# Optimization experiments

Measured on AMD Instinct MI355X. Metric: run time of the kernel, lower is better.

Reference implementation:

```python
import jax, jax.numpy as jnp
import numpy as np

B, T, H, P, ND = 32768, 128, 32, 7, 8
TEMPERATURE = 1.0
EPS = 1e-20


def setup_inputs() -> dict:
    key = jax.random.key(0)
    ks = jax.random.split(key, 12)
    sc = 0.1
    return {
        "h_n": jax.random.normal(ks[0], (1, B, H), dtype=jnp.float32),
        "c_n": jax.random.normal(ks[1], (1, B, H), dtype=jnp.float32),
        "noise": jax.random.normal(ks[2], (B, ND), dtype=jnp.float32),
        "gumbel_u": jax.random.uniform(ks[3], (T, B, P), dtype=jnp.float32),
        "W_init": jax.random.normal(ks[4], (H, H + ND), dtype=jnp.float32) * sc,
        "b_init": jnp.zeros((H,), dtype=jnp.float32),
        "W_ih": jax.random.normal(ks[5], (4 * H, P), dtype=jnp.float32) * sc,
        "W_hh": jax.random.normal(ks[6], (4 * H, H), dtype=jnp.float32) * sc,
        "b_ih": jnp.zeros((4 * H,), dtype=jnp.float32),
        "b_hh": jnp.zeros((4 * H,), dtype=jnp.float32),
        "W_head": jax.random.normal(ks[7], (P, H), dtype=jnp.float32) * sc,
        "b_head": jnp.zeros((P,), dtype=jnp.float32),
        "future_length": T,
    }


def reference(h_n, c_n, noise, gumbel_u, W_init, b_init, W_ih, W_hh, b_ih, b_hh, W_head, b_head, future_length):
    # fc_init on [h_n ; noise]
    h0 = jnp.concatenate([h_n[0], noise], axis=1) @ W_init.T + b_init  # (B, H)
    c0 = c_n[0]  # (B, H)
    nP = W_head.shape[0]
    y0 = jnp.zeros((h0.shape[0], nP), dtype=h0.dtype)

    def step(carry, u):
        h, c, y = carry
        # torch LSTM gate order: i, f, g, o
        gates = y @ W_ih.T + b_ih + h @ W_hh.T + b_hh  # (B, 4H)
        i, f, g, o = jnp.split(gates, 4, axis=-1)
        c = jax.nn.sigmoid(f) * c + jax.nn.sigmoid(i) * jnp.tanh(g)
        h = jax.nn.sigmoid(o) * jnp.tanh(c)
        logits = h @ W_head.T + b_head  # (B, P)
        # Gumbel-softmax (training, hard=True, straight-through)
        gnoise = -jnp.log(-jnp.log(u + EPS) + EPS)
        y_soft = jax.nn.softmax((logits + gnoise) / TEMPERATURE, axis=-1)
        y_hard = jax.nn.one_hot(jnp.argmax(y_soft, axis=-1), nP, dtype=y_soft.dtype)
        y = jax.lax.stop_gradient(y_hard - y_soft) + y_soft
        return (h, c, y), (logits, y)

    _, (logits_t, samples_t) = jax.lax.scan(step, (h0, c0, y0), gumbel_u)
    # (T, B, P) -> (B, T, P)
    return jnp.swapaxes(logits_t, 0, 1), jnp.swapaxes(samples_t, 0, 1)
```

## Files before the change

### kernel.cpp

```cpp
#include <hip/hip_runtime.h>


#define Hh 32
#define Pp 7
#define NDd 8

typedef float f32x2 __attribute__((ext_vector_type(2)));

static __device__ __forceinline__ f32x2 fma2(f32x2 w, float h, f32x2 a) {
  return __builtin_elementwise_fma(w, (f32x2){h, h}, a);
}

__global__ void gumbel_noise_kernel(const float4* __restrict__ u,
                                    float4* __restrict__ o, int n4) {
  int i = blockIdx.x * blockDim.x + threadIdx.x;
  int stride = gridDim.x * blockDim.x;
  for (; i < n4; i += stride) {
    float4 v = u[i];
    float4 r;
    r.x = -logf(-logf(v.x + 1e-20f) + 1e-20f);
    r.y = -logf(-logf(v.y + 1e-20f) + 1e-20f);
    r.z = -logf(-logf(v.z + 1e-20f) + 1e-20f);
    r.w = -logf(-logf(v.w + 1e-20f) + 1e-20f);
    o[i] = r;
  }
}

template <int PRE>
__global__ __launch_bounds__(64, 4) void gen_decoder_kernel(
    const float* __restrict__ h_n, const float* __restrict__ c_n,
    const float* __restrict__ noise, const float* __restrict__ gsrc,
    const float* __restrict__ W_init, const float* __restrict__ b_init,
    const float* __restrict__ W_ih, const float* __restrict__ W_hh,
    const float* __restrict__ b_ih, const float* __restrict__ b_hh,
    const float* __restrict__ W_head, const float* __restrict__ b_head,
    float* __restrict__ out, int B, int T)
{
  __shared__ f32x2 sTIG[8 * 32];
  __shared__ f32x2 sTFO[8 * 32];
  __shared__ __align__(16) float sm_h[2 * 36];
  __shared__ __align__(16) float smL[2][56];
  __shared__ __align__(16) float smS[2][56];

  const int l    = threadIdx.x;
  const int half = l >> 5;
  const int j    = l & 31;
  const int b    = blockIdx.x * 2 + half;

  for (int i = l; i < 8 * 32; i += 64) {
    int k = i >> 5, jj = i & 31;
    float vi = b_ih[jj]      + b_hh[jj]      + ((k < 7) ? W_ih[jj * 7 + k]        : 0.f);
    float vf = b_ih[32 + jj] + b_hh[32 + jj] + ((k < 7) ? W_ih[(32 + jj) * 7 + k] : 0.f);
    float vg = b_ih[64 + jj] + b_hh[64 + jj] + ((k < 7) ? W_ih[(64 + jj) * 7 + k] : 0.f);
    float vo = b_ih[96 + jj] + b_hh[96 + jj] + ((k < 7) ? W_ih[(96 + jj) * 7 + k] : 0.f);
    sTIG[i] = (f32x2){vi, vg};
    sTFO[i] = (f32x2){vf, vo};
  }

  {
    float x[Hh + NDd];
#pragma unroll
    for (int i = 0; i < 8; i++)
      ((float4*)x)[i] = *(const float4*)&h_n[(size_t)b * Hh + 4 * i];
    ((float4*)x)[8] = *(const float4*)&noise[(size_t)b * NDd];
    ((float4*)x)[9] = *(const float4*)&noise[(size_t)b * NDd + 4];
    float a = b_init[j];
    const float* wr = &W_init[j * (Hh + NDd)];
#pragma unroll
    for (int k = 0; k < Hh + NDd; k++) a = fmaf(wr[k], x[k], a);
    sm_h[half * 36 + j] = a;
  }
  float c = c_n[(size_t)b * Hh + j];

  f32x2 wPK[32];
  {
    const float* WA = W_hh + (size_t)l * Hh;
    const float* WB = W_hh + (size_t)(l + 64) * Hh;
#pragma unroll
    for (int kc = 0; kc < 8; kc++) {
      float4 wa = *(const float4*)&WA[4 * kc];
      float4 wb = *(const float4*)&WB[4 * kc];
      wPK[4 * kc + 0] = (f32x2){wa.x, wb.x};
      wPK[4 * kc + 1] = (f32x2){wa.y, wb.y};
      wPK[4 * kc + 2] = (f32x2){wa.z, wb.z};
      wPK[4 * kc + 3] = (f32x2){wa.w, wb.w};
    }
  }
  const f32x2* tbl = half ? sTFO : sTIG;

  const int hp = (l & 31) >> 2;
  const int hq = l & 3;
  float whead[8];
  float bh = 0.f;
  if (hp < 7) {
#pragma unroll
    for (int m = 0; m < 8; m++) whead[m] = W_head[hp * Hh + hq + 4 * m];
    bh = b_head[hp];
  } else {
#pragma unroll
    for (int m = 0; m < 8; m++) whead[m] = 0.f;
  }

  const int r7 = l & 7;
  const int cpc = (r7 < 7) ? r7 : 6;
  const float* gL = gsrc + (size_t)b * Pp + cpc;
  const size_t strideT = (size_t)B * Pp;
  const size_t SOFF = (size_t)B * T * Pp;

  int kA = 7, kB = 7;
  float* outL = out + (size_t)b * T * Pp;

  for (int t = 0; t < T; ++t) {
    float nv;
    if constexpr (PRE) {
      nv = gL[(size_t)t * strideT];
    } else {
      float uv = gL[(size_t)t * strideT];
      nv = -logf(-logf(uv + 1e-20f) + 1e-20f);
    }

    f32x2 accA = tbl[(kA << 5) + j];
    f32x2 accB = tbl[(kB << 5) + j];
#pragma unroll
    for (int kc = 0; kc < 8; kc++) {
      float4 hvA = *(const float4*)&sm_h[4 * kc];
      float4 hvB = *(const float4*)&sm_h[36 + 4 * kc];
      accA = fma2(wPK[4 * kc + 0], hvA.x, accA);
      accB = fma2(wPK[4 * kc + 0], hvB.x, accB);
      accA = fma2(wPK[4 * kc + 1], hvA.y, accA);
      accB = fma2(wPK[4 * kc + 1], hvB.y, accB);
      accA = fma2(wPK[4 * kc + 2], hvA.z, accA);
      accB = fma2(wPK[4 * kc + 2], hvB.z, accB);
      accA = fma2(wPK[4 * kc + 3], hvA.w, accA);
      accB = fma2(wPK[4 * kc + 3], hvB.w, accB);
    }

    float xAx = __shfl_xor(accA.x, 32), xAy = __shfl_xor(accA.y, 32);
    float xBx = __shfl_xor(accB.x, 32), xBy = __shfl_xor(accB.y, 32);
    float i_pre = (l < 32) ? accA.x : xBx;
    float g_pre = (l < 32) ? accA.y : xBy;
    float f_pre = (l < 32) ? xAx : accB.x;
    float o_pre = (l < 32) ? xAy : accB.y;

    float ig = 1.f / (1.f + expf(-i_pre));
    float fg = 1.f / (1.f + expf(-f_pre));
    float gg = tanhf(g_pre);
    float og = 1.f / (1.f + expf(-o_pre));
    float cc = fg * c + ig * gg;
    c = cc;
    float hj = og * tanhf(cc);
    sm_h[half * 36 + j] = hj;

    float lgp = 0.f;
    if (hp < 7) {
#pragma unroll
      for (int m = 0; m < 8; m++)
        lgp = fmaf(whead[m], sm_h[half * 36 + hq + 4 * m], lgp);
      lgp += __shfl_xor(lgp, 1);
      lgp += __shfl_xor(lgp, 2);
      lgp += bh;
    }

    float Lr = __shfl(lgp, (l & 32) + 4 * cpc);

    float bestv = (r7 < 7) ? (Lr + nv) : -__builtin_inff();
    int besti = r7;
#pragma unroll
    for (int mask = 1; mask <= 4; mask <<= 1) {
      float ov = __shfl_xor(bestv, mask);
      int   oi = __shfl_xor(besti, mask);
      if (ov > bestv || (ov == bestv && oi < besti)) { bestv = ov; besti = oi; }
    }
    kA = __shfl(besti, 0);
    kB = __shfl(besti, 32);
    int kme = (l < 32) ? kA : kB;

    if (hp < 7 && hq == 0) {
      int t8 = (t & 7) * Pp + hp;
      smL[half][t8] = lgp;
      smS[half][t8] = (kme == hp) ? 1.f : 0.f;
    }

    if ((t & 7) == 7) {
      int r = l & 31;
      if (r < 14) {
        size_t o = (size_t)(t - 7) * Pp + 4 * r;
        *(float4*)&outL[o]        = *(const float4*)&smL[half][4 * r];
        *(float4*)&outL[o + SOFF] = *(const float4*)&smS[half][4 * r];
      }
    } else if (t == T - 1) {
      int t0 = t & ~7;
      int cnt = (t - t0 + 1) * Pp;
      for (int i = l & 31; i < cnt; i += 32) {
        size_t o = (size_t)t0 * Pp + i;
        outL[o]        = smL[half][i];
        outL[o + SOFF] = smS[half][i];
      }
    }
  }
}

extern "C" void kernel_launch(void* const* d_in, const int* in_sizes, int n_in,
                              void* d_out, int out_size, void* d_ws, size_t ws_size,
                              hipStream_t stream) {
  const float* h_n     = (const float*)d_in[0];
  const float* c_n     = (const float*)d_in[1];
  const float* noise   = (const float*)d_in[2];
  const float* gumbel  = (const float*)d_in[3];
  const float* W_init  = (const float*)d_in[4];
  const float* b_init  = (const float*)d_in[5];
  const float* W_ih    = (const float*)d_in[6];
  const float* W_hh    = (const float*)d_in[7];
  const float* b_ih    = (const float*)d_in[8];
  const float* b_hh    = (const float*)d_in[9];
  const float* W_head  = (const float*)d_in[10];
  const float* b_head  = (const float*)d_in[11];

  int B = in_sizes[0] / Hh;
  int n = in_sizes[3];
  int T = n / (B * Pp);
  size_t nbytes = (size_t)n * sizeof(float);
  bool pre = (ws_size >= nbytes) && (n % 4 == 0);

  if (pre) {
    gumbel_noise_kernel<<<2048, 256, 0, stream>>>(
        (const float4*)gumbel, (float4*)d_ws, n / 4);
    gen_decoder_kernel<1><<<dim3(B / 2), dim3(64), 0, stream>>>(
        h_n, c_n, noise, (const float*)d_ws, W_init, b_init, W_ih, W_hh,
        b_ih, b_hh, W_head, b_head, (float*)d_out, B, T);
  } else {
    gen_decoder_kernel<0><<<dim3(B / 2), dim3(64), 0, stream>>>(
        h_n, c_n, noise, gumbel, W_init, b_init, W_ih, W_hh,
        b_ih, b_hh, W_head, b_head, (float*)d_out, B, T);
  }
}
```

Measured before the change: 986.2 us.

## Process four batch rows per wavefront to reuse register-resident W_hh

Each 64-thread block now handles four batch rows instead of two, so the W_hh weights held in registers are reused across four recurrent matvecs per timestep and the grid is halved. Gate nonlinearities, the head projection and the Gumbel argmax are each computed twice per lane, with the argmax lanes split into groups of 16. This gives more independent work per wavefront to hide latency and amortizes the weight loads. The cost is more registers and a longer serial chain per step, with half as many blocks available to fill the GPU.

```diff
diff --git a/kernel.cpp b/kernel.cpp
--- a/kernel.cpp
+++ b/kernel.cpp
@@ -38,14 +38,16 @@
 {
   __shared__ f32x2 sTIG[8 * 32];
   __shared__ f32x2 sTFO[8 * 32];
-  __shared__ __align__(16) float sm_h[2 * 36];
-  __shared__ __align__(16) float smL[2][56];
-  __shared__ __align__(16) float smS[2][56];
+  __shared__ __align__(16) float sm_h[4 * 36];
+  __shared__ __align__(16) float smL[4][56];
+  __shared__ __align__(16) float smS[4][56];
 
   const int l    = threadIdx.x;
   const int half = l >> 5;
   const int j    = l & 31;
-  const int b    = blockIdx.x * 2 + half;
+  const int b0   = blockIdx.x * 4;
+  const int bF   = b0 + half;
+  const int bS   = b0 + 2 + half;
 
   for (int i = l; i < 8 * 32; i += 64) {
     int k = i >> 5, jj = i & 31;
@@ -61,16 +63,30 @@
     float x[Hh + NDd];
 #pragma unroll
     for (int i = 0; i < 8; i++)
-      ((float4*)x)[i] = *(const float4*)&h_n[(size_t)b * Hh + 4 * i];
-    ((float4*)x)[8] = *(const float4*)&noise[(size_t)b * NDd];
-    ((float4*)x)[9] = *(const float4*)&noise[(size_t)b * NDd + 4];
+      ((float4*)x)[i] = *(const float4*)&h_n[(size_t)bF * Hh + 4 * i];
+    ((float4*)x)[8] = *(const float4*)&noise[(size_t)bF * NDd];
+    ((float4*)x)[9] = *(const float4*)&noise[(size_t)bF * NDd + 4];
     float a = b_init[j];
     const float* wr = &W_init[j * (Hh + NDd)];
 #pragma unroll
     for (int k = 0; k < Hh + NDd; k++) a = fmaf(wr[k], x[k], a);
     sm_h[half * 36 + j] = a;
   }
-  float c = c_n[(size_t)b * Hh + j];
+  {
+    float x[Hh + NDd];
+#pragma unroll
+    for (int i = 0; i < 8; i++)
+      ((float4*)x)[i] = *(const float4*)&h_n[(size_t)bS * Hh + 4 * i];
+    ((float4*)x)[8] = *(const float4*)&noise[(size_t)bS * NDd];
+    ((float4*)x)[9] = *(const float4*)&noise[(size_t)bS * NDd + 4];
+    float a = b_init[j];
+    const float* wr = &W_init[j * (Hh + NDd)];
+#pragma unroll
+    for (int k = 0; k < Hh + NDd; k++) a = fmaf(wr[k], x[k], a);
+    sm_h[(2 + half) * 36 + j] = a;
+  }
+  float cF = c_n[(size_t)bF * Hh + j];
+  float cS = c_n[(size_t)bS * Hh + j];
 
   f32x2 wPK[32];
   {
@@ -101,14 +117,16 @@
     for (int m = 0; m < 8; m++) whead[m] = 0.f;
   }
 
-  const int r7 = l & 7;
-  const int cpc = (r7 < 7) ? r7 : 6;
-  const float* gL = gsrc + (size_t)b * Pp + cpc;
+  const int g16 = l >> 4;
+  const int cp  = l & 15;
+  const int cpc = (cp < 7) ? cp : 6;
+  const float* gL = gsrc + (size_t)(b0 + g16) * Pp + cpc;
   const size_t strideT = (size_t)B * Pp;
   const size_t SOFF = (size_t)B * T * Pp;
 
-  int kA = 7, kB = 7;
-  float* outL = out + (size_t)b * T * Pp;
+  int k0 = 7, k1 = 7, k2 = 7, k3 = 7;
+  float* outF = out + (size_t)bF * T * Pp;
+  float* outS_ = out + (size_t)bS * T * Pp;
 
   for (int t = 0; t < T; ++t) {
     float nv;
@@ -119,82 +137,127 @@
       nv = -logf(-logf(uv + 1e-20f) + 1e-20f);
     }
 
-    f32x2 accA = tbl[(kA << 5) + j];
-    f32x2 accB = tbl[(kB << 5) + j];
+    f32x2 a0 = tbl[(k0 << 5) + j];
+    f32x2 a1 = tbl[(k1 << 5) + j];
+    f32x2 a2 = tbl[(k2 << 5) + j];
+    f32x2 a3 = tbl[(k3 << 5) + j];
 #pragma unroll
     for (int kc = 0; kc < 8; kc++) {
-      float4 hvA = *(const float4*)&sm_h[4 * kc];
-      float4 hvB = *(const float4*)&sm_h[36 + 4 * kc];
-      accA = fma2(wPK[4 * kc + 0], hvA.x, accA);
-      accB = fma2(wPK[4 * kc + 0], hvB.x, accB);
-      accA = fma2(wPK[4 * kc + 1], hvA.y, accA);
-      accB = fma2(wPK[4 * kc + 1], hvB.y, accB);
-      accA = fma2(wPK[4 * kc + 2], hvA.z, accA);
-      accB = fma2(wPK[4 * kc + 2], hvB.z, accB);
-      accA = fma2(wPK[4 * kc + 3], hvA.w, accA);
-      accB = fma2(wPK[4 * kc + 3], hvB.w, accB);
-    }
-
-    float xAx = __shfl_xor(accA.x, 32), xAy = __shfl_xor(accA.y, 32);
-    float xBx = __shfl_xor(accB.x, 32), xBy = __shfl_xor(accB.y, 32);
-    float i_pre = (l < 32) ? accA.x : xBx;
-    float g_pre = (l < 32) ? accA.y : xBy;
-    float f_pre = (l < 32) ? xAx : accB.x;
-    float o_pre = (l < 32) ? xAy : accB.y;
-
-    float ig = 1.f / (1.f + expf(-i_pre));
-    float fg = 1.f / (1.f + expf(-f_pre));
-    float gg = tanhf(g_pre);
-    float og = 1.f / (1.f + expf(-o_pre));
-    float cc = fg * c + ig * gg;
-    c = cc;
-    float hj = og * tanhf(cc);
-    sm_h[half * 36 + j] = hj;
-
-    float lgp = 0.f;
+      float4 h0v = *(const float4*)&sm_h[0 * 36 + 4 * kc];
+      float4 h1v = *(const float4*)&sm_h[1 * 36 + 4 * kc];
+      float4 h2v = *(const float4*)&sm_h[2 * 36 + 4 * kc];
+      float4 h3v = *(const float4*)&sm_h[3 * 36 + 4 * kc];
+      a0 = fma2(wPK[4 * kc + 0], h0v.x, a0);
+      a1 = fma2(wPK[4 * kc + 0], h1v.x, a1);
+      a2 = fma2(wPK[4 * kc + 0], h2v.x, a2);
+      a3 = fma2(wPK[4 * kc + 0], h3v.x, a3);
+      a0 = fma2(wPK[4 * kc + 1], h0v.y, a0);
+      a1 = fma2(wPK[4 * kc + 1], h1v.y, a1);
+      a2 = fma2(wPK[4 * kc + 1], h2v.y, a2);
+      a3 = fma2(wPK[4 * kc + 1], h3v.y, a3);
+      a0 = fma2(wPK[4 * kc + 2], h0v.z, a0);
+      a1 = fma2(wPK[4 * kc + 2], h1v.z, a1);
+      a2 = fma2(wPK[4 * kc + 2], h2v.z, a2);
+      a3 = fma2(wPK[4 * kc + 2], h3v.z, a3);
+      a0 = fma2(wPK[4 * kc + 3], h0v.w, a0);
+      a1 = fma2(wPK[4 * kc + 3], h1v.w, a1);
+      a2 = fma2(wPK[4 * kc + 3], h2v.w, a2);
+      a3 = fma2(wPK[4 * kc + 3], h3v.w, a3);
+    }
+
+    float x0x = __shfl_xor(a0.x, 32), x0y = __shfl_xor(a0.y, 32);
+    float x1x = __shfl_xor(a1.x, 32), x1y = __shfl_xor(a1.y, 32);
+    float x2x = __shfl_xor(a2.x, 32), x2y = __shfl_xor(a2.y, 32);
+    float x3x = __shfl_xor(a3.x, 32), x3y = __shfl_xor(a3.y, 32);
+    const bool lo = (l < 32);
+    float iF = lo ? a0.x : x1x;
+    float gF = lo ? a0.y : x1y;
+    float fF = lo ? x0x : a1.x;
+    float oF = lo ? x0y : a1.y;
+    float iS = lo ? a2.x : x3x;
+    float gS = lo ? a2.y : x3y;
+    float fS = lo ? x2x : a3.x;
+    float oS = lo ? x2y : a3.y;
+
+    float igF = 1.f / (1.f + expf(-iF));
+    float fgF = 1.f / (1.f + expf(-fF));
+    float ggF = tanhf(gF);
+    float ogF = 1.f / (1.f + expf(-oF));
+    float igS = 1.f / (1.f + expf(-iS));
+    float fgS = 1.f / (1.f + expf(-fS));
+    float ggS = tanhf(gS);
+    float ogS = 1.f / (1.f + expf(-oS));
+    float ccF = fgF * cF + igF * ggF;
+    float ccS = fgS * cS + igS * ggS;
+    cF = ccF;
+    cS = ccS;
+    float hjF = ogF * tanhf(ccF);
+    float hjS = ogS * tanhf(ccS);
+    sm_h[half * 36 + j] = hjF;
+    sm_h[(2 + half) * 36 + j] = hjS;
+
+    float lgF = 0.f, lgS = 0.f;
     if (hp < 7) {
 #pragma unroll
       for (int m = 0; m < 8; m++)
-        lgp = fmaf(whead[m], sm_h[half * 36 + hq + 4 * m], lgp);
-      lgp += __shfl_xor(lgp, 1);
-      lgp += __shfl_xor(lgp, 2);
-      lgp += bh;
-    }
-
-    float Lr = __shfl(lgp, (l & 32) + 4 * cpc);
-
-    float bestv = (r7 < 7) ? (Lr + nv) : -__builtin_inff();
-    int besti = r7;
+        lgF = fmaf(whead[m], sm_h[half * 36 + hq + 4 * m], lgF);
+      lgF += __shfl_xor(lgF, 1);
+      lgF += __shfl_xor(lgF, 2);
+      lgF += bh;
+#pragma unroll
+      for (int m = 0; m < 8; m++)
+        lgS = fmaf(whead[m], sm_h[(2 + half) * 36 + hq + 4 * m], lgS);
+      lgS += __shfl_xor(lgS, 1);
+      lgS += __shfl_xor(lgS, 2);
+      lgS += bh;
+    }
+
+    int srcq = ((g16 & 1) << 5) + 4 * cpc;
+    float LrF = __shfl(lgF, srcq);
+    float LrS = __shfl(lgS, srcq);
+    float Lr = (g16 < 2) ? LrF : LrS;
+
+    float bestv = (cp < 7) ? (Lr + nv) : -__builtin_inff();
+    int besti = cp;
 #pragma unroll
     for (int mask = 1; mask <= 4; mask <<= 1) {
       float ov = __shfl_xor(bestv, mask);
       int   oi = __shfl_xor(besti, mask);
       if (ov > bestv || (ov == bestv && oi < besti)) { bestv = ov; besti = oi; }
     }
-    kA = __shfl(besti, 0);
-    kB = __shfl(besti, 32);
-    int kme = (l < 32) ? kA : kB;
+    k0 = __shfl(besti, 0);
+    k1 = __shfl(besti, 16);
+    k2 = __shfl(besti, 32);
+    k3 = __shfl(besti, 48);
 
     if (hp < 7 && hq == 0) {
       int t8 = (t & 7) * Pp + hp;
-      smL[half][t8] = lgp;
-      smS[half][t8] = (kme == hp) ? 1.f : 0.f;
+      int kF = half ? k1 : k0;
+      int kS2 = half ? k3 : k2;
+      smL[half][t8] = lgF;
+      smS[half][t8] = (kF == hp) ? 1.f : 0.f;
+      smL[2 + half][t8] = lgS;
+      smS[2 + half][t8] = (kS2 == hp) ? 1.f : 0.f;
     }
 
     if ((t & 7) == 7) {
       int r = l & 31;
       if (r < 14) {
         size_t o = (size_t)(t - 7) * Pp + 4 * r;
-        *(float4*)&outL[o]        = *(const float4*)&smL[half][4 * r];
-        *(float4*)&outL[o + SOFF] = *(const float4*)&smS[half][4 * r];
+        *(float4*)&outF[o]         = *(const float4*)&smL[half][4 * r];
+        *(float4*)&outF[o + SOFF]  = *(const float4*)&smS[half][4 * r];
+        *(float4*)&outS_[o]        = *(const float4*)&smL[2 + half][4 * r];
+        *(float4*)&outS_[o + SOFF] = *(const float4*)&smS[2 + half][4 * r];
       }
     } else if (t == T - 1) {
       int t0 = t & ~7;
       int cnt = (t - t0 + 1) * Pp;
       for (int i = l & 31; i < cnt; i += 32) {
         size_t o = (size_t)t0 * Pp + i;
-        outL[o]        = smL[half][i];
-        outL[o + SOFF] = smS[half][i];
+        outF[o]         = smL[half][i];
+        outF[o + SOFF]  = smS[half][i];
+        outS_[o]        = smL[2 + half][i];
+        outS_[o + SOFF] = smS[2 + half][i];
       }
     }
   }
@@ -225,11 +288,11 @@
   if (pre) {
     gumbel_noise_kernel<<<2048, 256, 0, stream>>>(
         (const float4*)gumbel, (float4*)d_ws, n / 4);
-    gen_decoder_kernel<1><<<dim3(B / 2), dim3(64), 0, stream>>>(
+    gen_decoder_kernel<1><<<dim3(B / 4), dim3(64), 0, stream>>>(
         h_n, c_n, noise, (const float*)d_ws, W_init, b_init, W_ih, W_hh,
         b_ih, b_hh, W_head, b_head, (float*)d_out, B, T);
   } else {
-    gen_decoder_kernel<0><<<dim3(B / 2), dim3(64), 0, stream>>>(
+    gen_decoder_kernel<0><<<dim3(B / 4), dim3(64), 0, stream>>>(
         h_n, c_n, noise, gumbel, W_init, b_init, W_ih, W_hh,
         b_ih, b_hh, W_head, b_head, (float*)d_out, B, T);
   }
```

New measurement: 1.118 ms. 1.13x slower.

## Fuse Gumbel noise transform into decoder and prefetch next step's uniform

Applied to the files above, without the earlier changes.

Removes the separate Gumbel-noise precompute kernel and its workspace round trip. The decoder now computes -log(-log(u)) inline and software-prefetches the next timestep's uniform sample a step ahead to hide global load latency. It also drops the hp<7 branch around the head logit reduction (padded lanes have zero weights), which removes divergence. The trade is extra transcendental work inside the latency-bound recurrent loop.

```diff
diff --git a/kernel.cpp b/kernel.cpp
--- a/kernel.cpp
+++ b/kernel.cpp
@@ -11,22 +11,6 @@
   return __builtin_elementwise_fma(w, (f32x2){h, h}, a);
 }
 
-__global__ void gumbel_noise_kernel(const float4* __restrict__ u,
-                                    float4* __restrict__ o, int n4) {
-  int i = blockIdx.x * blockDim.x + threadIdx.x;
-  int stride = gridDim.x * blockDim.x;
-  for (; i < n4; i += stride) {
-    float4 v = u[i];
-    float4 r;
-    r.x = -logf(-logf(v.x + 1e-20f) + 1e-20f);
-    r.y = -logf(-logf(v.y + 1e-20f) + 1e-20f);
-    r.z = -logf(-logf(v.z + 1e-20f) + 1e-20f);
-    r.w = -logf(-logf(v.w + 1e-20f) + 1e-20f);
-    o[i] = r;
-  }
-}
-
-template <int PRE>
 __global__ __launch_bounds__(64, 4) void gen_decoder_kernel(
     const float* __restrict__ h_n, const float* __restrict__ c_n,
     const float* __restrict__ noise, const float* __restrict__ gsrc,
@@ -110,14 +94,13 @@
   int kA = 7, kB = 7;
   float* outL = out + (size_t)b * T * Pp;
 
+  float u_cur = gL[0];
+
   for (int t = 0; t < T; ++t) {
-    float nv;
-    if constexpr (PRE) {
-      nv = gL[(size_t)t * strideT];
-    } else {
-      float uv = gL[(size_t)t * strideT];
-      nv = -logf(-logf(uv + 1e-20f) + 1e-20f);
-    }
+    int tn = (t + 1 < T) ? (t + 1) : t;
+    float u_next = gL[(size_t)tn * strideT];
+
+    float nv = -logf(-logf(u_cur + 1e-20f) + 1e-20f);
 
     f32x2 accA = tbl[(kA << 5) + j];
     f32x2 accB = tbl[(kB << 5) + j];
@@ -152,14 +135,12 @@
     sm_h[half * 36 + j] = hj;
 
     float lgp = 0.f;
-    if (hp < 7) {
-#pragma unroll
-      for (int m = 0; m < 8; m++)
-        lgp = fmaf(whead[m], sm_h[half * 36 + hq + 4 * m], lgp);
-      lgp += __shfl_xor(lgp, 1);
-      lgp += __shfl_xor(lgp, 2);
-      lgp += bh;
-    }
+#pragma unroll
+    for (int m = 0; m < 8; m++)
+      lgp = fmaf(whead[m], sm_h[half * 36 + hq + 4 * m], lgp);
+    lgp += __shfl_xor(lgp, 1);
+    lgp += __shfl_xor(lgp, 2);
+    lgp += bh;
 
     float Lr = __shfl(lgp, (l & 32) + 4 * cpc);
 
@@ -197,6 +178,8 @@
         outL[o + SOFF] = smS[half][i];
       }
     }
+
+    u_cur = u_next;
   }
 }
 
@@ -219,18 +202,8 @@
   int B = in_sizes[0] / Hh;
   int n = in_sizes[3];
   int T = n / (B * Pp);
-  size_t nbytes = (size_t)n * sizeof(float);
-  bool pre = (ws_size >= nbytes) && (n % 4 == 0);
-
-  if (pre) {
-    gumbel_noise_kernel<<<2048, 256, 0, stream>>>(
-        (const float4*)gumbel, (float4*)d_ws, n / 4);
-    gen_decoder_kernel<1><<<dim3(B / 2), dim3(64), 0, stream>>>(
-        h_n, c_n, noise, (const float*)d_ws, W_init, b_init, W_ih, W_hh,
-        b_ih, b_hh, W_head, b_head, (float*)d_out, B, T);
-  } else {
-    gen_decoder_kernel<0><<<dim3(B / 2), dim3(64), 0, stream>>>(
-        h_n, c_n, noise, gumbel, W_init, b_init, W_ih, W_hh,
-        b_ih, b_hh, W_head, b_head, (float*)d_out, B, T);
-  }
+
+  gen_decoder_kernel<<<dim3(B / 2), dim3(64), 0, stream>>>(
+      h_n, c_n, noise, gumbel, W_init, b_init, W_ih, W_hh,
+      b_ih, b_hh, W_head, b_head, (float*)d_out, B, T);
 }
```

Result: no change. 971.7 us (-1.5%).
